# Kernel optimization log

Hardware: AMD Instinct MI355X
Metric: run time of the kernel (lower is better)

The kernel has to match this reference:

```python
import jax, jax.numpy as jnp
import numpy as np

HEADS = 8
DIM_HEAD = 64
SCALE = DIM_HEAD ** -0.5


def setup_inputs() -> dict:
    key = jax.random.key(0)
    k1, k2, k3 = jax.random.split(key, 3)
    b, seq, dim = 4, 8192, 512
    inner = HEADS * DIM_HEAD  # 512
    x = jax.random.normal(k1, (b, seq, dim), dtype=jnp.float32)
    w_qkv = jax.random.normal(k2, (dim, 3 * inner), dtype=jnp.float32) * (dim ** -0.5)
    w_out = jax.random.normal(k3, (inner, dim), dtype=jnp.float32) * (inner ** -0.5)
    b_out = jnp.zeros((dim,), dtype=jnp.float32)
    return {"x": x, "w_qkv": w_qkv, "w_out": w_out, "b_out": b_out, "f": 32}


def reference(x, w_qkv, w_out, b_out, f):
    b, seq, dim = x.shape
    h, dh = HEADS, DIM_HEAD
    n_sp = seq // f  # spatial tokens per frame

    qkv = jnp.einsum('bnd,de->bne', x, w_qkv)  # [b, seq, 3*inner]
    q, k, v = jnp.split(qkv, 3, axis=-1)

    def to_axial(t):
        # 'b n (h d) -> (b h) n d' then 'b (f n) d -> (b f) n d'
        t = t.reshape(b, seq, h, dh).transpose(0, 2, 1, 3)  # [b, h, seq, dh]
        return t.reshape(b * h * f, n_sp, dh)               # [(b h f), n_sp, dh]

    q = to_axial(q) * SCALE
    k = to_axial(k)
    v = to_axial(v)

    sim = jnp.einsum('bid,bjd->bij', q, k)      # [(b h f), n_sp, n_sp]
    attn = jax.nn.softmax(sim, axis=-1)
    out = jnp.einsum('bij,bjd->bid', attn, v)   # [(b h f), n_sp, dh]

    # reverse: '(b f) n d -> b (f n) d' then '(b h) n d -> b n (h d)'
    out = out.reshape(b, h, seq, dh).transpose(0, 2, 1, 3).reshape(b, seq, h * dh)
    return jnp.einsum('bne,ed->bnd', out, w_out) + b_out
```

## Files before the change

kernel.cpp:

```cpp
#include <hip/hip_runtime.h>
#include <hip/hip_bf16.h>
#include <cstdint>

using bf16x8 = __attribute__((ext_vector_type(8))) short;
using f32x4  = __attribute__((ext_vector_type(4))) float;
using f32x16 = __attribute__((ext_vector_type(16))) float;

typedef const __attribute__((address_space(1))) void* gas_ptr;
typedef __attribute__((address_space(3))) void* lds_ptr;

#define M_ROWS 32768
#define PLANE ((size_t)M_ROWS * 64)

__device__ __forceinline__ short f2bf(float f) {
  unsigned u = __builtin_bit_cast(unsigned, f);
  u += 0x7fffu + ((u >> 16) & 1u);
  return (short)(u >> 16);
}

__device__ __forceinline__ unsigned pack2(float a, float b) {
  unsigned ua = __builtin_bit_cast(unsigned, a);
  ua += 0x7fffu + ((ua >> 16) & 1u);
  unsigned ub = __builtin_bit_cast(unsigned, b);
  ub += 0x7fffu + ((ub >> 16) & 1u);
  return (ua >> 16) | (ub & 0xffff0000u);
}

__global__ __launch_bounds__(256) void convert_bf16(const float* __restrict__ src,
                                                    short* __restrict__ dst, int n8) {
  int i = blockIdx.x * 256 + threadIdx.x;
  if (i >= n8) return;
  const float4* s = (const float4*)(src + (size_t)i * 8);
  float4 a = s[0], b = s[1];
  uint4 o;
  o.x = pack2(a.x, a.y); o.y = pack2(a.z, a.w);
  o.z = pack2(b.x, b.y); o.w = pack2(b.z, b.w);
  *(uint4*)(dst + (size_t)i * 8) = o;
}

__global__ __launch_bounds__(256) void transpose_to_bf16(const float* __restrict__ src,
                                                         short* __restrict__ dst,
                                                         int R, int C) {
  int idx = blockIdx.x * 256 + threadIdx.x;
  if (idx >= R * C) return;
  int c = idx / R;
  int r = idx - c * R;
  dst[(size_t)c * R + r] = f2bf(src[(size_t)r * C + c]);
}

template <int MODE>
__device__ __forceinline__ void gemm8p_body(const short* __restrict__ A,
                                            const short* __restrict__ Bt,
                                            void* __restrict__ Cp,
                                            const float* __restrict__ bias,
                                            int Mt, int Nt, int N) {
  constexpr int K = 512;
  __shared__ short lds[32768];

  const int tid  = threadIdx.x;
  const int lane = tid & 63;
  const int w    = tid >> 6;
  const int c16  = lane & 15;
  const int g    = lane >> 4;
  const int wm   = w >> 2;
  const int wn   = w & 3;

  const int nwg = gridDim.x;
  const int bid = blockIdx.x;
  const int swz = (bid & 7) * (nwg >> 3) + (bid >> 3);
  const int mtile = swz / Nt;
  const int ntile = swz % Nt;
  const int m0 = mtile * 256;
  const int n0 = ntile * 256;

  const int stg_r = w * 16 + (lane >> 2);
  const int stg_c = ((lane & 3) ^ ((lane >> 3) & 3)) * 8;
  const short* gA = (MODE == 1)
      ? A + (size_t)(m0 + stg_r) * 64 + stg_c
      : A + (size_t)(m0 + stg_r) * K + stg_c;
  const short* gB = Bt + (size_t)(n0 + stg_r) * K + stg_c;
  short* const ldsA = lds;
  short* const ldsB = lds + 16384;
  const int stg_d = w * 512;

  const int f_lane = c16 * 32 + ((g ^ ((c16 >> 1) & 3)) * 8);

  f32x4 acc[2][4][4] = {};
  bf16x8 bf[4], af[4];

#define STGA_(st) do {                                                            \
    short* _d = ldsA + ((st) & 1) * 8192 + stg_d;                                 \
    if (MODE == 1) {                                                              \
      const short* _s = gA + (size_t)((st) >> 1) * PLANE + ((st) & 1) * 32;       \
      __builtin_amdgcn_global_load_lds((gas_ptr)_s, (lds_ptr)_d, 16, 0, 0);       \
      __builtin_amdgcn_global_load_lds((gas_ptr)(_s + 128 * 64), (lds_ptr)(_d + 4096), 16, 0, 0); \
    } else {                                                                      \
      const short* _s = gA + ((st) >> 1) * 64 + ((st) & 1) * 32;                  \
      __builtin_amdgcn_global_load_lds((gas_ptr)_s, (lds_ptr)_d, 16, 0, 0);       \
      __builtin_amdgcn_global_load_lds((gas_ptr)(_s + 128 * K), (lds_ptr)(_d + 4096), 16, 0, 0); \
    }                                                                             \
  } while (0)

#define STGB_(st) do {                                                            \
    const short* _s = gB + ((st) >> 1) * 64 + ((st) & 1) * 32;                    \
    short* _d = ldsB + ((st) & 1) * 8192 + stg_d;                                 \
    __builtin_amdgcn_global_load_lds((gas_ptr)_s, (lds_ptr)_d, 16, 0, 0);         \
    __builtin_amdgcn_global_load_lds((gas_ptr)(_s + 128 * K), (lds_ptr)(_d + 4096), 16, 0, 0); \
  } while (0)

#define MFMA_(mq) do {                                                            \
    __builtin_amdgcn_s_setprio(1);                                                \
    _Pragma("unroll")                                                             \
    for (int mf = 0; mf < 4; mf++)                                                \
      _Pragma("unroll")                                                           \
      for (int nf = 0; nf < 4; nf++)                                              \
        acc[mq][mf][nf] = __builtin_amdgcn_mfma_f32_16x16x32_bf16(af[mf], bf[nf], \
                                                      acc[mq][mf][nf], 0, 0, 0);  \
    __builtin_amdgcn_s_setprio(0);                                                \
  } while (0)

#define PH0_(s, st) do {                                                          \
    _Pragma("unroll")                                                             \
    for (int nf = 0; nf < 4; nf++)                                                \
      bf[nf] = *(const bf16x8*)&ldsB[(s) * 8192 + (wn * 64 + nf * 16) * 32 + f_lane]; \
    _Pragma("unroll")                                                             \
    for (int mf = 0; mf < 4; mf++)                                                \
      af[mf] = *(const bf16x8*)&ldsA[(s) * 8192 + (wm * 128 + mf * 16) * 32 + f_lane]; \
    STGA_(st);                                                                    \
    asm volatile("" ::: "memory");                                                \
    __builtin_amdgcn_s_barrier();                                                 \
    MFMA_(0);                                                                     \
    asm volatile("" ::: "memory");                                                \
    __builtin_amdgcn_s_barrier();                                                 \
    asm volatile("" ::: "memory");                                                \
  } while (0)

#define PH1_(s, st) do {                                                          \
    _Pragma("unroll")                                                             \
    for (int mf = 0; mf < 4; mf++)                                                \
      af[mf] = *(const bf16x8*)&ldsA[(s) * 8192 + (wm * 128 + 64 + mf * 16) * 32 + f_lane]; \
    STGB_(st);                                                                    \
    asm volatile("" ::: "memory");                                                \
    __builtin_amdgcn_s_barrier();                                                 \
    MFMA_(1);                                                                     \
    asm volatile("s_waitcnt vmcnt(0)" ::: "memory");                              \
    asm volatile("" ::: "memory");                                                \
    __builtin_amdgcn_s_barrier();                                                 \
    asm volatile("" ::: "memory");                                                \
  } while (0)

  STGA_(0); STGB_(0);
  asm volatile("s_waitcnt vmcnt(0)" ::: "memory");
  __builtin_amdgcn_s_barrier();
  asm volatile("" ::: "memory");

  for (int jj = 0; jj < 8; jj++) {
    const int te = 2 * jj;
    const int to = te + 1;
    const int sn = (to + 1 < 16) ? to + 1 : 15;
    PH0_(0, to);
    PH1_(0, to);
    PH0_(1, sn);
    PH1_(1, sn);
  }
#undef PH0_
#undef PH1_
#undef MFMA_
#undef STGA_
#undef STGB_

  asm volatile("s_waitcnt vmcnt(0)" ::: "memory");
  __builtin_amdgcn_s_barrier();

  if (MODE == 0) {
    #pragma unroll
    for (int p = 0; p < 2; p++) {
      if (p) __syncthreads();
      #pragma unroll
      for (int mf = 0; mf < 4; mf++)
        #pragma unroll
        for (int nf = 0; nf < 4; nf++) {
          const int lr  = wm * 64 + mf * 16 + g * 4;
          const int col = wn * 64 + nf * 16 + c16;
          #pragma unroll
          for (int r = 0; r < 4; r++)
            lds[(lr + r) * 256 + col] = f2bf(acc[p][mf][nf][r]);
        }
      __syncthreads();
      #pragma unroll
      for (int cg = 0; cg < 4; cg++) {
        const int colbase = n0 + cg * 64;
        const int plane = (colbase >> 9) * 8 + ((colbase >> 6) & 7);
        short* op = (short*)Cp + (size_t)plane * PLANE;
        #pragma unroll
        for (int it = 0; it < 2; it++) {
          const int lr  = it * 64 + (tid >> 3);
          const int sc8 = (tid & 7) * 8;
          const int grow = m0 + (lr >> 6) * 128 + p * 64 + (lr & 63);
          *(uint4*)(op + (size_t)grow * 64 + sc8) =
              *(const uint4*)&lds[lr * 256 + cg * 64 + sc8];
        }
      }
    }
  } else {
    #pragma unroll
    for (int mq = 0; mq < 2; mq++) {
      #pragma unroll
      for (int mf = 0; mf < 4; mf++) {
        #pragma unroll
        for (int nf = 0; nf < 4; nf++) {
          const int row = m0 + wm * 128 + mq * 64 + mf * 16 + g * 4;
          const int col = n0 + wn * 64 + nf * 16 + c16;
          float* C = (float*)Cp;
          const float bb = bias ? bias[col] : 0.f;
          #pragma unroll
          for (int r = 0; r < 4; r++)
            C[(size_t)(row + r) * N + col] = acc[mq][mf][nf][r] + bb;
        }
      }
    }
  }
}

__global__ __launch_bounds__(512, 2) void gemm8p_qkv(const short* __restrict__ A,
                                                     const short* __restrict__ Bt,
                                                     void* __restrict__ Cp,
                                                     int Mt, int Nt, int N) {
  gemm8p_body<0>(A, Bt, Cp, nullptr, Mt, Nt, N);
}
__global__ __launch_bounds__(512, 2) void gemm8p_out(const short* __restrict__ A,
                                                     const short* __restrict__ Bt,
                                                     void* __restrict__ Cp,
                                                     const float* __restrict__ bias,
                                                     int Mt, int Nt, int N) {
  gemm8p_body<1>(A, Bt, Cp, bias, Mt, Nt, N);
}

__global__ __launch_bounds__(512, 2) void attn_kernel(const short* __restrict__ qkv,
                                                      short* __restrict__ attn_out) {
  __shared__ short Kl[256 * 64];
  __shared__ short Vr[256 * 64];

  const int tid    = threadIdx.x;
  const int lane   = tid & 63;
  const int w      = tid >> 6;
  const int lane31 = lane & 31;
  const int hi     = lane >> 5;

  const int bid = blockIdx.x;
  const int fr  = bid & 31;
  const int h   = (bid >> 5) & 7;
  const int bb  = bid >> 8;
  const size_t rowbase = (size_t)bb * 8192 + (size_t)fr * 256;
  const short* qp = qkv + (size_t)(0 + h) * PLANE + rowbase * 64;
  const short* kp = qkv + (size_t)(8 + h) * PLANE + rowbase * 64;
  const short* vp = qkv + (size_t)(16 + h) * PLANE + rowbase * 64;

  #pragma unroll
  for (int j = 0; j < 4; j++) {
    const int g  = j * 512 + tid;
    const int r  = g >> 3;
    const int sl = g & 7;
    const int off = r * 128 + ((sl ^ (r & 7)) << 4);
    uint4 kc = *(const uint4*)(kp + (size_t)g * 8);
    *(uint4*)((char*)Kl + off) = kc;
    uint4 vc = *(const uint4*)(vp + (size_t)g * 8);
    *(uint4*)((char*)Vr + off) = vc;
  }
  __syncthreads();

  {
    const int p   = tid & 127;
    const int grp = tid >> 7;
    const int r0 = 2 * p, r1 = 2 * p + 1;
    bf16x8 ta[2], tb[2];
    #pragma unroll
    for (int i = 0; i < 2; i++) {
      const int cb = grp * 32 + i * 16;
      ta[i] = *(const bf16x8*)((const char*)Vr + r0 * 128 + (cb ^ ((r0 & 7) << 4)));
      tb[i] = *(const bf16x8*)((const char*)Vr + r1 * 128 + (cb ^ ((r1 & 7) << 4)));
    }
    __syncthreads();
    #pragma unroll
    for (int i = 0; i < 2; i++) {
      #pragma unroll
      for (int k = 0; k < 8; k++) {
        const int d = grp * 16 + i * 8 + k;
        unsigned pk = ((unsigned)(unsigned short)ta[i][k]) |
                      (((unsigned)(unsigned short)tb[i][k]) << 16);
        *(unsigned*)((char*)Vr + d * 512 + ((4 * p) ^ ((d & 7) << 4))) = pk;
      }
    }
  }
  __syncthreads();

  const int swl = (lane31 & 7) << 4;
  const int q0  = w * 32;
  unsigned pko[16];

  {
    const short* qrow = qp + (size_t)(q0 + lane31) * 64;
    bf16x8 qf[4];
    #pragma unroll
    for (int ds = 0; ds < 4; ds++)
      qf[ds] = *(const bf16x8*)(qrow + ds * 16 + 8 * hi);

    f32x16 o0 = {}, o1 = {};
    float m = 0.f, l = 0.f;

    #pragma unroll
    for (int j = 0; j < 4; j++) {
      f32x16 sA = {}, sB = {};
      __builtin_amdgcn_s_setprio(1);
      #pragma unroll
      for (int ds = 0; ds < 4; ds++) {
        bf16x8 kfA = *(const bf16x8*)((const char*)Kl + (j * 64 + lane31) * 128 +
                                      ((ds * 32 + 16 * hi) ^ swl));
        sA = __builtin_amdgcn_mfma_f32_32x32x16_bf16(kfA, qf[ds], sA, 0, 0, 0);
        bf16x8 kfB = *(const bf16x8*)((const char*)Kl + (j * 64 + 32 + lane31) * 128 +
                                      ((ds * 32 + 16 * hi) ^ swl));
        sB = __builtin_amdgcn_mfma_f32_32x32x16_bf16(kfB, qf[ds], sB, 0, 0, 0);
      }
      __builtin_amdgcn_s_setprio(0);

      float tm[16];
      #pragma unroll
      for (int r = 0; r < 16; r++) tm[r] = fmaxf(sA[r], sB[r]);
      #pragma unroll
      for (int st = 8; st > 0; st >>= 1)
        #pragma unroll
        for (int r = 0; r < 8; r++)
          if (r < st) tm[r] = fmaxf(tm[r], tm[r + st]);
      float bm = fmaxf(tm[0], __shfl_xor(tm[0], 32));

      if (j == 0) {
        m = bm;
      } else if (!__all((bm - m) <= 64.f)) {
        const float mnew = fmaxf(m, bm);
        const float corr = __expf((m - mnew) * 0.125f);
        #pragma unroll
        for (int r = 0; r < 16; r++) { o0[r] *= corr; o1[r] *= corr; }
        l *= corr;
        m = mnew;
      }

      float ts[16];
      #pragma unroll
      for (int r = 0; r < 16; r++) {
        sA[r] = __expf((sA[r] - m) * 0.125f);
        sB[r] = __expf((sB[r] - m) * 0.125f);
        ts[r] = sA[r] + sB[r];
      }
      #pragma unroll
      for (int st = 8; st > 0; st >>= 1)
        #pragma unroll
        for (int r = 0; r < 8; r++)
          if (r < st) ts[r] += ts[r + st];
      l += ts[0] + __shfl_xor(ts[0], 32);

#define PVBLK(SV, rb, mm) do {                                                     \
        unsigned u0 = pack2(SV[(rb) + 0], SV[(rb) + 1]);                           \
        unsigned u1 = pack2(SV[(rb) + 2], SV[(rb) + 3]);                           \
        unsigned u2 = pack2(SV[(rb) + 4], SV[(rb) + 5]);                           \
        unsigned u3 = pack2(SV[(rb) + 6], SV[(rb) + 7]);                           \
        int s0 = hi ? (int)u0 : (int)u2;                                           \
        int s1 = hi ? (int)u1 : (int)u3;                                           \
        int r0 = __shfl_xor(s0, 32);                                               \
        int r1 = __shfl_xor(s1, 32);                                               \
        int4 paw;                                                                  \
        paw.x = hi ? r0 : (int)u0;                                                 \
        paw.y = hi ? r1 : (int)u1;                                                 \
        paw.z = hi ? (int)u2 : r0;                                                 \
        paw.w = hi ? (int)u3 : r1;                                                 \
        bf16x8 pa = __builtin_bit_cast(bf16x8, paw);                               \
        bf16x8 v0f = *(const bf16x8*)((const char*)Vr + (size_t)lane31 * 512 +     \
                                      (((mm) * 32 + 16 * hi) ^ swl));              \
        bf16x8 v1f = *(const bf16x8*)((const char*)Vr + (size_t)(32 + lane31) * 512 + \
                                      (((mm) * 32 + 16 * hi) ^ swl));              \
        o0 = __builtin_amdgcn_mfma_f32_32x32x16_bf16(v0f, pa, o0, 0, 0, 0);        \
        o1 = __builtin_amdgcn_mfma_f32_32x32x16_bf16(v1f, pa, o1, 0, 0, 0);        \
      } while (0)

      PVBLK(sA, 0, j * 4 + 0);
      PVBLK(sA, 8, j * 4 + 1);
      PVBLK(sB, 0, j * 4 + 2);
      PVBLK(sB, 8, j * 4 + 3);
#undef PVBLK
    }

    const float inv = 1.0f / l;
    #pragma unroll
    for (int r = 0; r < 16; r++) { o0[r] *= inv; o1[r] *= inv; }
    #pragma unroll
    for (int g2 = 0; g2 < 4; g2++) {
      pko[2 * g2 + 0] = pack2(o0[4 * g2 + 0], o0[4 * g2 + 1]);
      pko[2 * g2 + 1] = pack2(o0[4 * g2 + 2], o0[4 * g2 + 3]);
      pko[8 + 2 * g2 + 0] = pack2(o1[4 * g2 + 0], o1[4 * g2 + 1]);
      pko[8 + 2 * g2 + 1] = pack2(o1[4 * g2 + 2], o1[4 * g2 + 3]);
    }
  }

  __syncthreads();
  {
    const int row = q0 + lane31;
    const int rx  = (row & 7) << 4;
    #pragma unroll
    for (int g2 = 0; g2 < 4; g2++) {
      uint2 a, b;
      a.x = pko[2 * g2 + 0]; a.y = pko[2 * g2 + 1];
      b.x = pko[8 + 2 * g2 + 0]; b.y = pko[8 + 2 * g2 + 1];
      *(uint2*)((char*)Kl + row * 128 + ((16 * g2 + 8 * hi) ^ rx))      = a;
      *(uint2*)((char*)Kl + row * 128 + ((64 + 16 * g2 + 8 * hi) ^ rx)) = b;
    }
  }
  __syncthreads();
  short* op = attn_out + (size_t)h * PLANE + rowbase * 64;
  #pragma unroll
  for (int j = 0; j < 4; j++) {
    const int row = j * 64 + (tid >> 3);
    const int sl  = tid & 7;
    uint4 v = *(const uint4*)((const char*)Kl + row * 128 + ((sl << 4) ^ ((row & 7) << 4)));
    *(uint4*)(op + (size_t)row * 64 + sl * 8) = v;
  }
}

extern "C" void kernel_launch(void* const* d_in, const int* in_sizes, int n_in,
                              void* d_out, int out_size, void* d_ws, size_t ws_size,
                              hipStream_t stream) {
  const float* x     = (const float*)d_in[0];
  const float* w_qkv = (const float*)d_in[1];
  const float* w_out = (const float*)d_in[2];
  const float* b_out = (const float*)d_in[3];
  float* out = (float*)d_out;

  const int M = M_ROWS, DIM = 512, NQKV = 1536;

  short* wqkvT = (short*)d_ws;
  short* woutT = wqkvT + (size_t)NQKV * DIM;
  short* qkvb  = woutT + (size_t)DIM * DIM;
  short* attnb = qkvb + (size_t)M * NQKV;
  short* xbf   = attnb;

  transpose_to_bf16<<<(DIM * NQKV + 255) / 256, 256, 0, stream>>>(w_qkv, wqkvT, DIM, NQKV);
  transpose_to_bf16<<<(DIM * DIM + 255) / 256, 256, 0, stream>>>(w_out, woutT, DIM, DIM);
  convert_bf16<<<(M * DIM / 8 + 255) / 256, 256, 0, stream>>>(x, xbf, M * DIM / 8);

  gemm8p_qkv<<<(M / 256) * (NQKV / 256), 512, 0, stream>>>(xbf, wqkvT, qkvb,
                                                           M / 256, NQKV / 256, NQKV);

  attn_kernel<<<1024, 512, 0, stream>>>(qkvb, attnb);

  gemm8p_out<<<(M / 256) * (DIM / 256), 512, 0, stream>>>(attnb, woutT, out, b_out,
                                                          M / 256, DIM / 256, DIM);
}
```

Before: 163.8 us.

## Replace QKV GEMM with 256x128-tile kernel at higher occupancy

Adds a dedicated QKV projection kernel that uses 256x128 output tiles, a single accumulator set per wave and a smaller LDS footprint, and raises launch bounds to four blocks per CU. The new kernel uses a simpler load/barrier/MFMA step schedule in place of the earlier phased pipeline, and the output GEMM keeps its specialised path. This doubles the grid and raises occupancy to hide latency and improve load balance across CUs. In exchange, each B tile is reused less, more A traffic is re-read, and there are more barriers per k-step.

```diff
diff --git a/kernel.cpp b/kernel.cpp
--- a/kernel.cpp
+++ b/kernel.cpp
@@ -48,12 +48,139 @@
   dst[(size_t)c * R + r] = f2bf(src[(size_t)r * C + c]);
 }
 
-template <int MODE>
-__device__ __forceinline__ void gemm8p_body(const short* __restrict__ A,
-                                            const short* __restrict__ Bt,
-                                            void* __restrict__ Cp,
-                                            const float* __restrict__ bias,
-                                            int Mt, int Nt, int N) {
+__global__ __launch_bounds__(512, 4) void gemm_qkv2(const short* __restrict__ A,
+                                                    const short* __restrict__ Bt,
+                                                    short* __restrict__ Cp,
+                                                    int Mt, int Nt, int N) {
+  constexpr int K = 512;
+  __shared__ short lds[24576];
+
+  const int tid  = threadIdx.x;
+  const int lane = tid & 63;
+  const int w    = tid >> 6;
+  const int c16  = lane & 15;
+  const int g    = lane >> 4;
+  const int wm   = w >> 1;
+  const int wn   = w & 1;
+
+  const int nwg = gridDim.x;
+  const int bid = blockIdx.x;
+  const int swz = (bid & 7) * (nwg >> 3) + (bid >> 3);
+  const int mtile = swz / Nt;
+  const int ntile = swz % Nt;
+  const int m0 = mtile * 256;
+  const int n0 = ntile * 128;
+
+  const int stg_r = w * 16 + (lane >> 2);
+  const int stg_c = ((lane & 3) ^ ((lane >> 3) & 3)) * 8;
+  const short* gA = A + (size_t)(m0 + stg_r) * K + stg_c;
+  const int stg_rB = tid >> 2;
+  const int stg_cB = ((tid & 3) ^ ((tid >> 3) & 3)) * 8;
+  const short* gB = Bt + (size_t)(n0 + stg_rB) * K + stg_cB;
+
+  short* const ldsA = lds;
+  short* const ldsB = lds + 16384;
+  const int stg_d = w * 512;
+
+  const int f_lane = c16 * 32 + ((g ^ ((c16 >> 1) & 3)) * 8);
+
+  f32x4 acc[4][4] = {};
+  bf16x8 bf[4], af[4];
+
+#define STGA_(st) do {                                                            \
+    short* _d = ldsA + ((st) & 1) * 8192 + stg_d;                                 \
+    const short* _s = gA + ((st) >> 1) * 64 + ((st) & 1) * 32;                    \
+    __builtin_amdgcn_global_load_lds((gas_ptr)_s, (lds_ptr)_d, 16, 0, 0);         \
+    __builtin_amdgcn_global_load_lds((gas_ptr)(_s + 128 * K), (lds_ptr)(_d + 4096), 16, 0, 0); \
+  } while (0)
+
+#define STGB_(st) do {                                                            \
+    short* _d = ldsB + ((st) & 1) * 4096 + stg_d;                                 \
+    const short* _s = gB + ((st) >> 1) * 64 + ((st) & 1) * 32;                    \
+    __builtin_amdgcn_global_load_lds((gas_ptr)_s, (lds_ptr)_d, 16, 0, 0);         \
+  } while (0)
+
+#define STEP_(s, st) do {                                                         \
+    _Pragma("unroll")                                                             \
+    for (int nf = 0; nf < 4; nf++)                                                \
+      bf[nf] = *(const bf16x8*)&ldsB[(s) * 4096 + (wn * 64 + nf * 16) * 32 + f_lane]; \
+    _Pragma("unroll")                                                             \
+    for (int mf = 0; mf < 4; mf++)                                                \
+      af[mf] = *(const bf16x8*)&ldsA[(s) * 8192 + (wm * 64 + mf * 16) * 32 + f_lane]; \
+    STGA_(st);                                                                    \
+    STGB_(st);                                                                    \
+    asm volatile("" ::: "memory");                                                \
+    __builtin_amdgcn_s_barrier();                                                 \
+    __builtin_amdgcn_s_setprio(1);                                                \
+    _Pragma("unroll")                                                             \
+    for (int mf = 0; mf < 4; mf++)                                                \
+      _Pragma("unroll")                                                           \
+      for (int nf = 0; nf < 4; nf++)                                              \
+        acc[mf][nf] = __builtin_amdgcn_mfma_f32_16x16x32_bf16(af[mf], bf[nf],     \
+                                                      acc[mf][nf], 0, 0, 0);      \
+    __builtin_amdgcn_s_setprio(0);                                                \
+    asm volatile("s_waitcnt vmcnt(0)" ::: "memory");                              \
+    asm volatile("" ::: "memory");                                                \
+    __builtin_amdgcn_s_barrier();                                                 \
+    asm volatile("" ::: "memory");                                                \
+  } while (0)
+
+  STGA_(0); STGB_(0);
+  asm volatile("s_waitcnt vmcnt(0)" ::: "memory");
+  __builtin_amdgcn_s_barrier();
+  asm volatile("" ::: "memory");
+
+  for (int jj = 0; jj < 8; jj++) {
+    const int t1 = 2 * jj + 1;
+    const int t2 = (2 * jj + 2 < 16) ? 2 * jj + 2 : 15;
+    STEP_(0, t1);
+    STEP_(1, t2);
+  }
+#undef STEP_
+#undef STGA_
+#undef STGB_
+
+  asm volatile("s_waitcnt vmcnt(0)" ::: "memory");
+  __builtin_amdgcn_s_barrier();
+
+  #pragma unroll
+  for (int p = 0; p < 2; p++) {
+    if (p) __syncthreads();
+    if ((wm >> 1) == p) {
+      #pragma unroll
+      for (int mf = 0; mf < 4; mf++)
+        #pragma unroll
+        for (int nf = 0; nf < 4; nf++) {
+          const int lr  = (wm & 1) * 64 + mf * 16 + g * 4;
+          const int col = wn * 64 + nf * 16 + c16;
+          #pragma unroll
+          for (int r = 0; r < 4; r++)
+            lds[(lr + r) * 128 + col] = f2bf(acc[mf][nf][r]);
+        }
+    }
+    __syncthreads();
+    #pragma unroll
+    for (int cg = 0; cg < 2; cg++) {
+      const int colbase = n0 + cg * 64;
+      const int plane = (colbase >> 9) * 8 + ((colbase >> 6) & 7);
+      short* op = Cp + (size_t)plane * PLANE;
+      #pragma unroll
+      for (int it = 0; it < 2; it++) {
+        const int lr  = it * 64 + (tid >> 3);
+        const int sc8 = (tid & 7) * 8;
+        const int grow = m0 + p * 128 + lr;
+        *(uint4*)(op + (size_t)grow * 64 + sc8) =
+            *(const uint4*)&lds[lr * 128 + cg * 64 + sc8];
+      }
+    }
+  }
+}
+
+__global__ __launch_bounds__(512, 2) void gemm8p_out(const short* __restrict__ A,
+                                                     const short* __restrict__ Bt,
+                                                     void* __restrict__ Cp,
+                                                     const float* __restrict__ bias,
+                                                     int Mt, int Nt, int N) {
   constexpr int K = 512;
   __shared__ short lds[32768];
 
@@ -75,9 +202,7 @@
 
   const int stg_r = w * 16 + (lane >> 2);
   const int stg_c = ((lane & 3) ^ ((lane >> 3) & 3)) * 8;
-  const short* gA = (MODE == 1)
-      ? A + (size_t)(m0 + stg_r) * 64 + stg_c
-      : A + (size_t)(m0 + stg_r) * K + stg_c;
+  const short* gA = A + (size_t)(m0 + stg_r) * 64 + stg_c;
   const short* gB = Bt + (size_t)(n0 + stg_r) * K + stg_c;
   short* const ldsA = lds;
   short* const ldsB = lds + 16384;
@@ -90,15 +215,9 @@
 
 #define STGA_(st) do {                                                            \
     short* _d = ldsA + ((st) & 1) * 8192 + stg_d;                                 \
-    if (MODE == 1) {                                                              \
-      const short* _s = gA + (size_t)((st) >> 1) * PLANE + ((st) & 1) * 32;       \
-      __builtin_amdgcn_global_load_lds((gas_ptr)_s, (lds_ptr)_d, 16, 0, 0);       \
-      __builtin_amdgcn_global_load_lds((gas_ptr)(_s + 128 * 64), (lds_ptr)(_d + 4096), 16, 0, 0); \
-    } else {                                                                      \
-      const short* _s = gA + ((st) >> 1) * 64 + ((st) & 1) * 32;                  \
-      __builtin_amdgcn_global_load_lds((gas_ptr)_s, (lds_ptr)_d, 16, 0, 0);       \
-      __builtin_amdgcn_global_load_lds((gas_ptr)(_s + 128 * K), (lds_ptr)(_d + 4096), 16, 0, 0); \
-    }                                                                             \
+    const short* _s = gA + (size_t)((st) >> 1) * PLANE + ((st) & 1) * 32;         \
+    __builtin_amdgcn_global_load_lds((gas_ptr)_s, (lds_ptr)_d, 16, 0, 0);         \
+    __builtin_amdgcn_global_load_lds((gas_ptr)(_s + 128 * 64), (lds_ptr)(_d + 4096), 16, 0, 0); \
   } while (0)
 
 #define STGB_(st) do {                                                            \
@@ -172,68 +291,22 @@
   asm volatile("s_waitcnt vmcnt(0)" ::: "memory");
   __builtin_amdgcn_s_barrier();
 
-  if (MODE == 0) {
-    #pragma unroll
-    for (int p = 0; p < 2; p++) {
-      if (p) __syncthreads();
-      #pragma unroll
-      for (int mf = 0; mf < 4; mf++)
+  #pragma unroll
+  for (int mq = 0; mq < 2; mq++) {
+    #pragma unroll
+    for (int mf = 0; mf < 4; mf++) {
+      #pragma unroll
+      for (int nf = 0; nf < 4; nf++) {
+        const int row = m0 + wm * 128 + mq * 64 + mf * 16 + g * 4;
+        const int col = n0 + wn * 64 + nf * 16 + c16;
+        float* C = (float*)Cp;
+        const float bb = bias ? bias[col] : 0.f;
         #pragma unroll
-        for (int nf = 0; nf < 4; nf++) {
-          const int lr  = wm * 64 + mf * 16 + g * 4;
-          const int col = wn * 64 + nf * 16 + c16;
-          #pragma unroll
-          for (int r = 0; r < 4; r++)
-            lds[(lr + r) * 256 + col] = f2bf(acc[p][mf][nf][r]);
-        }
-      __syncthreads();
-      #pragma unroll
-      for (int cg = 0; cg < 4; cg++) {
-        const int colbase = n0 + cg * 64;
-        const int plane = (colbase >> 9) * 8 + ((colbase >> 6) & 7);
-        short* op = (short*)Cp + (size_t)plane * PLANE;
-        #pragma unroll
-        for (int it = 0; it < 2; it++) {
-          const int lr  = it * 64 + (tid >> 3);
-          const int sc8 = (tid & 7) * 8;
-          const int grow = m0 + (lr >> 6) * 128 + p * 64 + (lr & 63);
-          *(uint4*)(op + (size_t)grow * 64 + sc8) =
-              *(const uint4*)&lds[lr * 256 + cg * 64 + sc8];
-        }
+        for (int r = 0; r < 4; r++)
+          C[(size_t)(row + r) * N + col] = acc[mq][mf][nf][r] + bb;
       }
     }
-  } else {
-    #pragma unroll
-    for (int mq = 0; mq < 2; mq++) {
-      #pragma unroll
-      for (int mf = 0; mf < 4; mf++) {
-        #pragma unroll
-        for (int nf = 0; nf < 4; nf++) {
-          const int row = m0 + wm * 128 + mq * 64 + mf * 16 + g * 4;
-          const int col = n0 + wn * 64 + nf * 16 + c16;
-          float* C = (float*)Cp;
-          const float bb = bias ? bias[col] : 0.f;
-          #pragma unroll
-          for (int r = 0; r < 4; r++)
-            C[(size_t)(row + r) * N + col] = acc[mq][mf][nf][r] + bb;
-        }
-      }
-    }
-  }
-}
-
-__global__ __launch_bounds__(512, 2) void gemm8p_qkv(const short* __restrict__ A,
-                                                     const short* __restrict__ Bt,
-                                                     void* __restrict__ Cp,
-                                                     int Mt, int Nt, int N) {
-  gemm8p_body<0>(A, Bt, Cp, nullptr, Mt, Nt, N);
-}
-__global__ __launch_bounds__(512, 2) void gemm8p_out(const short* __restrict__ A,
-                                                     const short* __restrict__ Bt,
-                                                     void* __restrict__ Cp,
-                                                     const float* __restrict__ bias,
-                                                     int Mt, int Nt, int N) {
-  gemm8p_body<1>(A, Bt, Cp, bias, Mt, Nt, N);
+  }
 }
 
 __global__ __launch_bounds__(512, 2) void attn_kernel(const short* __restrict__ qkv,
@@ -445,8 +518,8 @@
   transpose_to_bf16<<<(DIM * DIM + 255) / 256, 256, 0, stream>>>(w_out, woutT, DIM, DIM);
   convert_bf16<<<(M * DIM / 8 + 255) / 256, 256, 0, stream>>>(x, xbf, M * DIM / 8);
 
-  gemm8p_qkv<<<(M / 256) * (NQKV / 256), 512, 0, stream>>>(xbf, wqkvT, qkvb,
-                                                           M / 256, NQKV / 256, NQKV);
+  gemm_qkv2<<<(M / 256) * (NQKV / 128), 512, 0, stream>>>(xbf, wqkvT, qkvb,
+                                                          M / 256, NQKV / 128, NQKV);
 
   attn_kernel<<<1024, 512, 0, stream>>>(qkvb, attnb);
 
```

After: 169.4 us. 3.4% more time.
